# Kernel tuning notes

Hardware: AMD Instinct MI355X
Metric: run time of the kernel (lower is better)

Reference implementation:

```python
import jax, jax.numpy as jnp
import numpy as np

N = 50000          # nodes
E = 1_600_000      # directed edges (before self-loops)
F_IN = 256         # input features
HID = 32           # hidden channels
HEADS = 8
NUM_CLASSES = 40


def setup_inputs() -> dict:
    key = jax.random.key(0)
    ks = jax.random.split(key, 12)
    s = 0.1  # small init scale for numerical sanity
    return {
        "x": jax.random.normal(ks[0], (N, F_IN), jnp.float32),
        "edge_index": jax.random.randint(ks[1], (2, E), 0, N, dtype=jnp.int32),
        # layer 0: F_IN -> HID, heads=8, concat
        "W0": jax.random.normal(ks[2], (F_IN, HEADS * HID), jnp.float32) * s,
        "as0": jax.random.normal(ks[3], (HEADS, HID), jnp.float32) * s,
        "ad0": jax.random.normal(ks[4], (HEADS, HID), jnp.float32) * s,
        "b0": jnp.zeros((HEADS * HID,), jnp.float32),
        # layer 1: 8*HID -> 8*HID, heads=1, concat
        "W1": jax.random.normal(ks[5], (HEADS * HID, HEADS * HID), jnp.float32) * s,
        "as1": jax.random.normal(ks[6], (1, HEADS * HID), jnp.float32) * s,
        "ad1": jax.random.normal(ks[7], (1, HEADS * HID), jnp.float32) * s,
        "b1": jnp.zeros((HEADS * HID,), jnp.float32),
        # layer 2: 8*HID -> NUM_CLASSES, heads=1, concat=False (mean == identity for 1 head)
        "W2": jax.random.normal(ks[8], (HEADS * HID, NUM_CLASSES), jnp.float32) * s,
        "as2": jax.random.normal(ks[9], (1, NUM_CLASSES), jnp.float32) * s,
        "ad2": jax.random.normal(ks[10], (1, NUM_CLASSES), jnp.float32) * s,
        "b2": jnp.zeros((NUM_CLASSES,), jnp.float32),
    }


def _gat_conv(x, src, dst, W, att_src, att_dst, bias, heads, out_ch, concat):
    """PyG GATConv (eval mode, self-loops already included in src/dst)."""
    n = x.shape[0]
    xp = (x @ W).reshape(n, heads, out_ch)                # [N,H,C]
    a_src = jnp.einsum("nhc,hc->nh", xp, att_src)          # [N,H]
    a_dst = jnp.einsum("nhc,hc->nh", xp, att_dst)          # [N,H]
    e = jax.nn.leaky_relu(a_src[src] + a_dst[dst], 0.2)    # [Etot,H]
    # segment softmax over incoming edges of each destination node
    m = jax.ops.segment_max(e, dst, num_segments=n)        # [N,H]
    ex = jnp.exp(e - m[dst])
    denom = jax.ops.segment_sum(ex, dst, num_segments=n)   # [N,H]
    alpha = ex / denom[dst]                                # [Etot,H]
    msg = xp[src] * alpha[:, :, None]                      # [Etot,H,C]
    out = jax.ops.segment_sum(msg, dst, num_segments=n)    # [N,H,C]
    out = out.reshape(n, heads * out_ch) if concat else out.mean(axis=1)
    return out + bias


def reference(x, edge_index, W0, as0, ad0, b0, W1, as1, ad1, b1, W2, as2, ad2, b2):
    loops = jnp.arange(N, dtype=edge_index.dtype)
    src = jnp.concatenate([edge_index[0], loops])  # add self-loops (PyG default)
    dst = jnp.concatenate([edge_index[1], loops])
    h = _gat_conv(x, src, dst, W0, as0, ad0, b0, HEADS, HID, True)
    h = jax.nn.elu(h)  # dropout p=0.6 is identity in eval mode
    h = _gat_conv(h, src, dst, W1, as1, ad1, b1, 1, HEADS * HID, True)
    h = jax.nn.elu(h)
    x1 = _gat_conv(h, src, dst, W2, as2, ad2, b2, 1, NUM_CLASSES, False)
    return jax.nn.log_softmax(x1, axis=1)  # original returns log_softmax of last conv output
```

## Files before the change

### kernel.cpp

```cpp
#include <hip/hip_runtime.h>
#include <hip/hip_bf16.h>

#define N_NODES 50000
#define N_EDGES 1600000
#define ETOT (N_EDGES + N_NODES)
#define NP 50048
#define NBUCK 196

typedef __attribute__((ext_vector_type(8))) short short8;
typedef __attribute__((ext_vector_type(4))) float f32x4;
typedef __attribute__((ext_vector_type(2))) float f32x2;

__device__ __forceinline__ float b2f(unsigned short u) {
    union { unsigned int i; float f; } v; v.i = ((unsigned int)u) << 16; return v.f;
}
__device__ __forceinline__ unsigned short f2b(float f) {
    union { float f; unsigned int i; } v; v.f = f;
    unsigned int r = v.i + 0x7FFF + ((v.i >> 16) & 1);
    return (unsigned short)(r >> 16);
}
__device__ __forceinline__ unsigned char f2q(float f) {
    int r = __builtin_amdgcn_cvt_pk_fp8_f32(f, f, 0, false);
    return (unsigned char)(r & 0xFF);
}

__global__ void k_tb(const float* __restrict__ W, unsigned short* __restrict__ Wt,
                     int K, int C) {
    int idx = blockIdx.x * 256 + threadIdx.x;
    if (idx >= K * C) return;
    int k = idx / C, c = idx - k * C;
    Wt[c * K + k] = f2b(W[idx]);
}

__global__ __launch_bounds__(256) void k_mku0(const float* __restrict__ W,
                                              const float* __restrict__ attS,
                                              const float* __restrict__ attD,
                                              unsigned short* __restrict__ u0t) {
    int lane = threadIdx.x & 63;
    int k = blockIdx.x * 4 + (threadIdx.x >> 6);
    if (k >= 256) return;
    int h = lane >> 3, c0 = lane & 7;
    const float* wr = W + (size_t)k * 256 + h * 32;
    float ss = 0.f, sd = 0.f;
    #pragma unroll
    for (int t = 0; t < 4; ++t) {
        int c = c0 + t * 8;
        float w = wr[c];
        ss += w * attS[h * 32 + c];
        sd += w * attD[h * 32 + c];
    }
    #pragma unroll
    for (int off = 1; off < 8; off <<= 1) {
        ss += __shfl_xor(ss, off);
        sd += __shfl_xor(sd, off);
    }
    if (c0 == 0) {
        u0t[(size_t)h * 256 + k] = f2b(ss);
        u0t[(size_t)(8 + h) * 256 + k] = f2b(sd);
    }
}

__global__ __launch_bounds__(256) void k_mku1(const float* __restrict__ W,
                                              const float* __restrict__ attS,
                                              const float* __restrict__ attD,
                                              float* __restrict__ u, int C) {
    int lane = threadIdx.x & 63;
    int k = blockIdx.x * 4 + (threadIdx.x >> 6);
    if (k >= 256) return;
    const float* wr = W + (size_t)k * C;
    float ss = 0.f, sd = 0.f;
    for (int c = lane; c < C; c += 64) {
        float w = wr[c];
        ss += w * attS[c];
        sd += w * attD[c];
    }
    #pragma unroll
    for (int off = 32; off > 0; off >>= 1) {
        ss += __shfl_xor(ss, off);
        sd += __shfl_xor(sd, off);
    }
    if (lane == 0) { u[k * 2] = ss; u[k * 2 + 1] = sd; }
}

__global__ __launch_bounds__(256) void k_bcount(const int* __restrict__ ei,
                                                int* __restrict__ bcnt) {
    __shared__ int h[NBUCK];
    for (int i = threadIdx.x; i < NBUCK; i += 256) h[i] = 0;
    __syncthreads();
    int e0 = blockIdx.x * 4096, e1 = min(e0 + 4096, ETOT);
    for (int e = e0 + threadIdx.x; e < e1; e += 256) {
        int dst = (e < N_EDGES) ? ei[N_EDGES + e] : (e - N_EDGES);
        atomicAdd(&h[dst >> 8], 1);
    }
    __syncthreads();
    for (int i = threadIdx.x; i < NBUCK; i += 256)
        if (h[i]) atomicAdd(&bcnt[i], h[i]);
}

__global__ void k_bscan(const int* __restrict__ bcnt, int* __restrict__ bstart,
                        int* __restrict__ bcursor) {
    __shared__ int tmp[256];
    int t = threadIdx.x;
    int v = (t < NBUCK) ? bcnt[t] : 0;
    tmp[t] = v;
    __syncthreads();
    for (int off = 1; off < 256; off <<= 1) {
        int u = (t >= off) ? tmp[t - off] : 0;
        __syncthreads();
        tmp[t] += u;
        __syncthreads();
    }
    int ex = tmp[t] - v;
    if (t < NBUCK) { bstart[t] = ex; bcursor[t] = ex; }
    if (t == 0) bstart[NBUCK] = ETOT;
}

__global__ __launch_bounds__(256) void k_bscatter(const int* __restrict__ ei,
                                                  int* __restrict__ bcursor,
                                                  unsigned int* __restrict__ stage) {
    __shared__ int h[NBUCK], base[NBUCK], cur[NBUCK], gbase[NBUCK];
    __shared__ int tmp[256];
    __shared__ unsigned int buf[8192];
    int t = threadIdx.x;
    for (int i = t; i < NBUCK; i += 256) h[i] = 0;
    __syncthreads();
    int e0 = blockIdx.x * 8192, e1 = min(e0 + 8192, ETOT);
    for (int e = e0 + t; e < e1; e += 256) {
        int dst = (e < N_EDGES) ? ei[N_EDGES + e] : (e - N_EDGES);
        atomicAdd(&h[dst >> 8], 1);
    }
    __syncthreads();
    int v = (t < NBUCK) ? h[t] : 0;
    tmp[t] = v;
    __syncthreads();
    for (int off = 1; off < 256; off <<= 1) {
        int u = (t >= off) ? tmp[t - off] : 0;
        __syncthreads();
        tmp[t] += u;
        __syncthreads();
    }
    if (t < NBUCK) { base[t] = tmp[t] - v; cur[t] = tmp[t] - v; }
    __syncthreads();
    for (int e = e0 + t; e < e1; e += 256) {
        int src, dst;
        if (e < N_EDGES) { src = ei[e]; dst = ei[N_EDGES + e]; }
        else             { src = dst = e - N_EDGES; }
        int b = dst >> 8;
        int p = atomicAdd(&cur[b], 1);
        buf[p] = ((unsigned int)b << 24) | ((unsigned int)src << 8) | (unsigned int)(dst & 255);
    }
    __syncthreads();
    if (t < NBUCK) gbase[t] = atomicAdd(&bcursor[t], h[t]);
    __syncthreads();
    int cnt = e1 - e0;
    for (int i = t; i < cnt; i += 256) {
        unsigned int pr = buf[i];
        int b = pr >> 24;
        stage[gbase[b] + (i - base[b])] = pr;
    }
}

__global__ __launch_bounds__(256) void k_csr(const unsigned int* __restrict__ stage,
                                             const int* __restrict__ bstart,
                                             int* __restrict__ rowptr, int* __restrict__ deg,
                                             unsigned short* __restrict__ csr) {
    __shared__ int cnt[256], cur[256], tmp[256];
    int b = blockIdx.x;
    int t = threadIdx.x;
    cnt[t] = 0;
    __syncthreads();
    int s0 = bstart[b], s1 = bstart[b + 1];
    for (int i = s0 + t; i < s1; i += 256)
        atomicAdd(&cnt[stage[i] & 255], 1);
    __syncthreads();
    int v = cnt[t];
    tmp[t] = v;
    __syncthreads();
    for (int off = 1; off < 256; off <<= 1) {
        int u = (t >= off) ? tmp[t - off] : 0;
        __syncthreads();
        tmp[t] += u;
        __syncthreads();
    }
    int ex = tmp[t] - v;
    int node = b * 256 + t;
    if (node < N_NODES) { rowptr[node] = s0 + ex; deg[node] = v; }
    cur[t] = s0 + ex;
    __syncthreads();
    for (int i = s0 + t; i < s1; i += 256) {
        unsigned int pr = stage[i];
        int p = atomicAdd(&cur[pr & 255], 1);
        csr[p] = (unsigned short)((pr >> 8) & 0xFFFF);
    }
}

template <bool ATT>
__global__ __launch_bounds__(256) void k_gemm_w(
    const unsigned short* __restrict__ A, const unsigned short* __restrict__ Bt,
    unsigned char* __restrict__ Cout,
    const unsigned short* __restrict__ But,
    float* __restrict__ Catt,
    int nrows, int ldc) {
    const int K = 256;
    int lane = threadIdx.x & 63;
    int wave = threadIdx.x >> 6;
    int row0 = blockIdx.x * 128 + wave * 32;
    int col0 = blockIdx.y * 128;
    bool doAtt = ATT && (blockIdx.y == 0);
    int ar0 = row0 + (lane & 15); if (ar0 >= nrows) ar0 = nrows - 1;
    int ar1 = row0 + 16 + (lane & 15); if (ar1 >= nrows) ar1 = nrows - 1;
    int ks = (lane >> 4) * 8;
    const unsigned short* Ap0 = A + (size_t)ar0 * K + ks;
    const unsigned short* Ap1 = A + (size_t)ar1 * K + ks;
    f32x4 acc[2][8];
    f32x4 aat[2] = {{0,0,0,0},{0,0,0,0}};
    #pragma unroll
    for (int rt = 0; rt < 2; ++rt)
        #pragma unroll
        for (int ct = 0; ct < 8; ++ct) acc[rt][ct] = {0, 0, 0, 0};
    for (int k = 0; k < K; k += 32) {
        short8 a0 = *(const short8*)(Ap0 + k);
        short8 a1 = *(const short8*)(Ap1 + k);
        #pragma unroll
        for (int ct = 0; ct < 8; ++ct) {
            short8 b = *(const short8*)(Bt + (size_t)(col0 + ct * 16 + (lane & 15)) * K + k + ks);
            acc[0][ct] = __builtin_amdgcn_mfma_f32_16x16x32_bf16(a0, b, acc[0][ct], 0, 0, 0);
            acc[1][ct] = __builtin_amdgcn_mfma_f32_16x16x32_bf16(a1, b, acc[1][ct], 0, 0, 0);
        }
        if (doAtt) {
            short8 b = *(const short8*)(But + (size_t)(lane & 15) * K + k + ks);
            aat[0] = __builtin_amdgcn_mfma_f32_16x16x32_bf16(a0, b, aat[0], 0, 0, 0);
            aat[1] = __builtin_amdgcn_mfma_f32_16x16x32_bf16(a1, b, aat[1], 0, 0, 0);
        }
    }
    int cb = lane & 15;
    #pragma unroll
    for (int rt = 0; rt < 2; ++rt) {
        int rbase = row0 + rt * 16 + (lane >> 4) * 4;
        #pragma unroll
        for (int ct = 0; ct < 8; ++ct) {
            int cc = col0 + ct * 16 + cb;
            #pragma unroll
            for (int j = 0; j < 4; ++j)
                Cout[(size_t)(rbase + j) * ldc + cc] = f2q(acc[rt][ct][j]);
        }
        if (doAtt) {
            #pragma unroll
            for (int j = 0; j < 4; ++j)
                Catt[(size_t)(rbase + j) * 16 + cb] = aat[rt][j];
        }
    }
}

__global__ __launch_bounds__(256) void k_gemm_b(
    const unsigned short* __restrict__ A, const unsigned short* __restrict__ Bt,
    unsigned char* __restrict__ Cout, int nrows, int ncols, int ldc) {
    const int K = 256;
    int lane = threadIdx.x & 63;
    int wave = threadIdx.x >> 6;
    int row0 = blockIdx.x * 128 + wave * 32;
    int ar0 = row0 + (lane & 15); if (ar0 >= nrows) ar0 = nrows - 1;
    int ar1 = row0 + 16 + (lane & 15); if (ar1 >= nrows) ar1 = nrows - 1;
    int ks = (lane >> 4) * 8;
    const unsigned short* Ap0 = A + (size_t)ar0 * K + ks;
    const unsigned short* Ap1 = A + (size_t)ar1 * K + ks;
    f32x4 acc[2][4] = {{{0,0,0,0},{0,0,0,0},{0,0,0,0},{0,0,0,0}},
                       {{0,0,0,0},{0,0,0,0},{0,0,0,0},{0,0,0,0}}};
    for (int k = 0; k < K; k += 32) {
        short8 a0 = *(const short8*)(Ap0 + k);
        short8 a1 = *(const short8*)(Ap1 + k);
        #pragma unroll
        for (int ct = 0; ct < 4; ++ct) {
            short8 b = *(const short8*)(Bt + (size_t)(ct * 16 + (lane & 15)) * K + k + ks);
            acc[0][ct] = __builtin_amdgcn_mfma_f32_16x16x32_bf16(a0, b, acc[0][ct], 0, 0, 0);
            acc[1][ct] = __builtin_amdgcn_mfma_f32_16x16x32_bf16(a1, b, acc[1][ct], 0, 0, 0);
        }
    }
    int cb = lane & 15;
    #pragma unroll
    for (int rt = 0; rt < 2; ++rt) {
        int rbase = row0 + rt * 16 + (lane >> 4) * 4;
        #pragma unroll
        for (int ct = 0; ct < 4; ++ct) {
            int cc = ct * 16 + cb;
            #pragma unroll
            for (int j = 0; j < 4; ++j) {
                float v = (cc < ncols) ? acc[rt][ct][j] : 0.f;
                Cout[(size_t)(rbase + j) * ldc + cc] = f2q(v);
            }
        }
    }
}

__global__ __launch_bounds__(256) void k_split(const float* __restrict__ x,
                                               unsigned short* __restrict__ xb) {
    int idx = blockIdx.x * 256 + threadIdx.x;
    if (idx >= N_NODES * 64) return;
    float4 v = *(const float4*)(x + (size_t)idx * 4);
    ushort4 w;
    w.x = f2b(v.x); w.y = f2b(v.y); w.z = f2b(v.z); w.w = f2b(v.w);
    *(ushort4*)(xb + (size_t)idx * 4) = w;
}

template <int H>
__global__ __launch_bounds__(256) void k_gatherq(
    const unsigned char* __restrict__ xq,
    const float* __restrict__ asrc, const float* __restrict__ adst,
    const int* __restrict__ rowptr, const int* __restrict__ deg,
    const unsigned short* __restrict__ csr,
    const float* __restrict__ bias,
    const float* __restrict__ un,
    unsigned short* __restrict__ o,
    float* __restrict__ asn, float* __restrict__ adn) {
    constexpr int SS = (H == 8) ? 16 : 1;
    int lane = threadIdx.x & 63;
    int node = blockIdx.x * 4 + (threadIdx.x >> 6);
    if (node >= N_NODES) return;
    int ptr = rowptr[node], dg = deg[node];
    int g = lane >> 4, l4 = lane & 15;
    int cbase = l4 * 16;
    int head = (H == 8) ? (l4 >> 1) : 0;
    float ad = adst[(size_t)node * SS + head];
    float acc[16];
    #pragma unroll
    for (int j = 0; j < 16; ++j) acc[j] = 0.f;
    float den = 0.f;
    int dge = (dg + 3) & ~3;
    int i = g;
    int ci = ptr + min(i, dg - 1);
    int sn0 = csr[ci];
    float e0 = asrc[(size_t)sn0 * SS + head];
    uint4 v0 = *(const uint4*)(xq + (size_t)sn0 * 256 + cbase);
    bool ok0 = (i < dg);
    while (i < dge) {
        int in = i + 4;
        int cn = ptr + min(in, dg - 1);
        int sn1 = csr[cn];
        float e1 = asrc[(size_t)sn1 * SS + head];
        uint4 v1 = *(const uint4*)(xq + (size_t)sn1 * 256 + cbase);
        float e = e0 + ad;
        e = (e >= 0.f) ? e : 0.2f * e;
        float a0 = ok0 ? __expf(fminf(e, 70.f)) : 0.f;
        den += a0;
        f32x2 f;
        f = __builtin_amdgcn_cvt_pk_f32_fp8(v0.x, false); acc[0] += a0 * f.x;  acc[1] += a0 * f.y;
        f = __builtin_amdgcn_cvt_pk_f32_fp8(v0.x, true);  acc[2] += a0 * f.x;  acc[3] += a0 * f.y;
        f = __builtin_amdgcn_cvt_pk_f32_fp8(v0.y, false); acc[4] += a0 * f.x;  acc[5] += a0 * f.y;
        f = __builtin_amdgcn_cvt_pk_f32_fp8(v0.y, true);  acc[6] += a0 * f.x;  acc[7] += a0 * f.y;
        f = __builtin_amdgcn_cvt_pk_f32_fp8(v0.z, false); acc[8] += a0 * f.x;  acc[9] += a0 * f.y;
        f = __builtin_amdgcn_cvt_pk_f32_fp8(v0.z, true);  acc[10] += a0 * f.x; acc[11] += a0 * f.y;
        f = __builtin_amdgcn_cvt_pk_f32_fp8(v0.w, false); acc[12] += a0 * f.x; acc[13] += a0 * f.y;
        f = __builtin_amdgcn_cvt_pk_f32_fp8(v0.w, true);  acc[14] += a0 * f.x; acc[15] += a0 * f.y;
        i = in; e0 = e1; v0 = v1; ok0 = (in < dg);
    }
    den += __shfl_xor(den, 16);
    den += __shfl_xor(den, 32);
    #pragma unroll
    for (int j = 0; j < 16; ++j) {
        acc[j] += __shfl_xor(acc[j], 16);
        acc[j] += __shfl_xor(acc[j], 32);
    }
    if (g) return;
    float inv = 1.0f / den;
    float sN = 0.f, dN = 0.f;
    short8 w0, w1;
    #pragma unroll
    for (int j = 0; j < 16; ++j) {
        int c = cbase + j;
        float v = acc[j] * inv + bias[c];
        v = (v > 0.f) ? v : (__expf(v) - 1.f);
        unsigned short bb = f2b(v);
        if (j < 8) w0[j] = (short)bb; else w1[j - 8] = (short)bb;
        sN += v * un[c * 2];
        dN += v * un[c * 2 + 1];
    }
    *(short8*)(o + (size_t)node * 256 + cbase) = w0;
    *(short8*)(o + (size_t)node * 256 + cbase + 8) = w1;
    #pragma unroll
    for (int off = 8; off > 0; off >>= 1) {
        sN += __shfl_xor(sN, off);
        dN += __shfl_xor(dN, off);
    }
    if (l4 == 0) { asn[node] = sN; adn[node] = dN; }
}

__global__ __launch_bounds__(256) void k_gf(
    const unsigned char* __restrict__ xq,
    const float* __restrict__ asrc, const float* __restrict__ adst,
    const int* __restrict__ rowptr, const int* __restrict__ deg,
    const unsigned short* __restrict__ csr,
    const float* __restrict__ bias,
    float* __restrict__ out) {
    int lane = threadIdx.x & 63;
    int node = blockIdx.x * 4 + (threadIdx.x >> 6);
    if (node >= N_NODES) return;
    int ptr = rowptr[node], dg = deg[node];
    int g = lane >> 3, l8 = lane & 7;
    int cbase = l8 * 8;
    float ad = adst[node];
    float acc[8] = {0,0,0,0,0,0,0,0};
    float den = 0.f;
    int dge = (dg + 7) & ~7;
    int i = g;
    int ci = ptr + min(i, dg - 1);
    int sn0 = csr[ci];
    float e0 = asrc[sn0];
    uint2 v0 = *(const uint2*)(xq + (size_t)sn0 * 64 + cbase);
    bool ok0 = (i < dg);
    while (i < dge) {
        int in = i + 8;
        int cn = ptr + min(in, dg - 1);
        int sn1 = csr[cn];
        float e1 = asrc[sn1];
        uint2 v1 = *(const uint2*)(xq + (size_t)sn1 * 64 + cbase);
        float e = e0 + ad;
        e = (e >= 0.f) ? e : 0.2f * e;
        float a0 = ok0 ? __expf(fminf(e, 70.f)) : 0.f;
        den += a0;
        f32x2 f;
        f = __builtin_amdgcn_cvt_pk_f32_fp8(v0.x, false); acc[0] += a0 * f.x; acc[1] += a0 * f.y;
        f = __builtin_amdgcn_cvt_pk_f32_fp8(v0.x, true);  acc[2] += a0 * f.x; acc[3] += a0 * f.y;
        f = __builtin_amdgcn_cvt_pk_f32_fp8(v0.y, false); acc[4] += a0 * f.x; acc[5] += a0 * f.y;
        f = __builtin_amdgcn_cvt_pk_f32_fp8(v0.y, true);  acc[6] += a0 * f.x; acc[7] += a0 * f.y;
        i = in; e0 = e1; v0 = v1; ok0 = (in < dg);
    }
    den += __shfl_xor(den, 8);
    den += __shfl_xor(den, 16);
    den += __shfl_xor(den, 32);
    #pragma unroll
    for (int j = 0; j < 8; ++j) {
        acc[j] += __shfl_xor(acc[j], 8);
        acc[j] += __shfl_xor(acc[j], 16);
        acc[j] += __shfl_xor(acc[j], 32);
    }
    if (g) return;
    float inv = 1.0f / den;
    float val[8], mx = -1e30f;
    #pragma unroll
    for (int j = 0; j < 8; ++j) {
        int c = cbase + j;
        val[j] = (c < 40) ? acc[j] * inv + bias[c] : -1e30f;
        mx = fmaxf(mx, val[j]);
    }
    #pragma unroll
    for (int off = 4; off > 0; off >>= 1) mx = fmaxf(mx, __shfl_xor(mx, off));
    float ex = 0.f;
    #pragma unroll
    for (int j = 0; j < 8; ++j) {
        int c = cbase + j;
        if (c < 40) ex += __expf(val[j] - mx);
    }
    #pragma unroll
    for (int off = 4; off > 0; off >>= 1) ex += __shfl_xor(ex, off);
    float lse = __logf(ex);
    #pragma unroll
    for (int j = 0; j < 8; ++j) {
        int c = cbase + j;
        if (c < 40) out[(size_t)node * 40 + c] = val[j] - mx - lse;
    }
}

extern "C" void kernel_launch(void* const* d_in, const int* in_sizes, int n_in,
                              void* d_out, int out_size, void* d_ws, size_t ws_size,
                              hipStream_t stream) {
    const float* x   = (const float*)d_in[0];
    const int*   ei  = (const int*)d_in[1];
    const float* W0  = (const float*)d_in[2];
    const float* as0 = (const float*)d_in[3];
    const float* ad0 = (const float*)d_in[4];
    const float* b0  = (const float*)d_in[5];
    const float* W1  = (const float*)d_in[6];
    const float* as1 = (const float*)d_in[7];
    const float* ad1 = (const float*)d_in[8];
    const float* b1  = (const float*)d_in[9];
    const float* W2  = (const float*)d_in[10];
    const float* as2 = (const float*)d_in[11];
    const float* ad2 = (const float*)d_in[12];
    const float* b2  = (const float*)d_in[13];
    float* out = (float*)d_out;

    char* p = (char*)d_ws;
    auto carve = [&](size_t bytes) -> char* {
        char* r = p; p += (bytes + 255) & ~(size_t)255; return r;
    };
    unsigned short* xb   = (unsigned short*)carve((size_t)NP * 256 * 2);
    unsigned short* xpb  = (unsigned short*)carve((size_t)NP * 256 * 2);
    unsigned short* h    = (unsigned short*)carve((size_t)NP * 256 * 2);
    unsigned char*  xq2  = (unsigned char*)carve((size_t)NP * 64);
    unsigned short* Wt0  = (unsigned short*)carve(256 * 256 * 2);
    unsigned short* Wt1  = (unsigned short*)carve(256 * 256 * 2);
    unsigned short* Wt2  = (unsigned short*)carve(64 * 256 * 2);
    unsigned short* u0t  = (unsigned short*)carve(16 * 256 * 2);
    float* att0 = (float*)carve((size_t)NP * 16 * 4);
    float* u1 = (float*)carve(256 * 2 * 4);
    float* u2 = (float*)carve(256 * 2 * 4);
    float* asrc1 = (float*)carve((size_t)N_NODES * 4);
    float* adst1 = (float*)carve((size_t)N_NODES * 4);
    float* asrc2 = (float*)carve((size_t)N_NODES * 4);
    float* adst2 = (float*)carve((size_t)N_NODES * 4);
    int* deg    = (int*)carve((size_t)N_NODES * 4);
    int* rowptr = (int*)carve((size_t)N_NODES * 4);
    int* bcnt   = (int*)carve((size_t)NBUCK * 4);
    int* bstart = (int*)carve((size_t)(NBUCK + 1) * 4);
    int* bcursor= (int*)carve((size_t)NBUCK * 4);
    unsigned int* stage = (unsigned int*)carve((size_t)ETOT * 4);
    unsigned short* csr = (unsigned short*)carve((size_t)ETOT * 2);
    unsigned char* xq = (unsigned char*)xpb;

    hipMemsetAsync(bcnt, 0, (size_t)NBUCK * 4, stream);
    hipMemsetAsync(Wt2, 0, 64 * 256 * 2, stream);

    k_tb<<<(256 * 256 + 255) / 256, 256, 0, stream>>>(W0, Wt0, 256, 256);
    k_tb<<<(256 * 256 + 255) / 256, 256, 0, stream>>>(W1, Wt1, 256, 256);
    k_tb<<<(256 * 40 + 255) / 256, 256, 0, stream>>>(W2, Wt2, 256, 40);

    k_mku0<<<64, 256, 0, stream>>>(W0, as0, ad0, u0t);
    k_mku1<<<64, 256, 0, stream>>>(W1, as1, ad1, u1, 256);
    k_mku1<<<64, 256, 0, stream>>>(W2, as2, ad2, u2, 40);

    k_bcount<<<(ETOT + 4095) / 4096, 256, 0, stream>>>(ei, bcnt);
    k_bscan<<<1, 256, 0, stream>>>(bcnt, bstart, bcursor);
    k_bscatter<<<(ETOT + 8191) / 8192, 256, 0, stream>>>(ei, bcursor, stage);
    k_csr<<<NBUCK, 256, 0, stream>>>(stage, bstart, rowptr, deg, csr);

    dim3 gg(NP / 128, 2);
    dim3 gn(N_NODES / 4);
    dim3 g1(NP / 128);
    k_split<<<(N_NODES * 64 + 255) / 256, 256, 0, stream>>>(x, xb);
    k_gemm_w<true><<<gg, 256, 0, stream>>>(xb, Wt0, xq, u0t, att0, N_NODES, 256);
    k_gatherq<8><<<gn, 256, 0, stream>>>(xq, att0, att0 + 8, rowptr, deg, csr,
                                         b0, u1, h, asrc1, adst1);
    k_gemm_w<false><<<gg, 256, 0, stream>>>(h, Wt1, xq, nullptr, nullptr, N_NODES, 256);
    k_gatherq<1><<<gn, 256, 0, stream>>>(xq, asrc1, adst1, rowptr, deg, csr,
                                         b1, u2, xb, asrc2, adst2);
    k_gemm_b<<<g1, 256, 0, stream>>>(xb, Wt2, xq2, N_NODES, 40, 64);
    k_gf<<<gn, 256, 0, stream>>>(xq2, asrc2, adst2, rowptr, deg, csr, b2, out);
}
```

Measured before the change: 412.1 us.

## Use fixed-capacity buckets to drop count/scan passes and merge setup kernels

```diff
diff --git a/kernel.cpp b/kernel.cpp
--- a/kernel.cpp
+++ b/kernel.cpp
@@ -6,6 +6,7 @@
 #define ETOT (N_EDGES + N_NODES)
 #define NP 50048
 #define NBUCK 196
+#define BCAP 16384
 
 typedef __attribute__((ext_vector_type(8))) short short8;
 typedef __attribute__((ext_vector_type(4))) float f32x4;
@@ -24,12 +25,24 @@
     return (unsigned char)(r & 0xFF);
 }
 
-__global__ void k_tb(const float* __restrict__ W, unsigned short* __restrict__ Wt,
-                     int K, int C) {
+__global__ void k_tb3(const float* __restrict__ W0, const float* __restrict__ W1,
+                      const float* __restrict__ W2,
+                      unsigned short* __restrict__ Wt0, unsigned short* __restrict__ Wt1,
+                      unsigned short* __restrict__ Wt2) {
     int idx = blockIdx.x * 256 + threadIdx.x;
-    if (idx >= K * C) return;
-    int k = idx / C, c = idx - k * C;
-    Wt[c * K + k] = f2b(W[idx]);
+    if (idx < 65536) {
+        int k = idx >> 8, c = idx & 255;
+        Wt0[c * 256 + k] = f2b(W0[idx]);
+    } else if (idx < 131072) {
+        int i = idx - 65536;
+        int k = i >> 8, c = i & 255;
+        Wt1[c * 256 + k] = f2b(W1[i]);
+    } else {
+        int i = idx - 131072;
+        if (i >= 16384) return;
+        int k = i >> 6, c = i & 63;
+        Wt2[c * 256 + k] = (c < 40) ? f2b(W2[k * 40 + c]) : 0;
+    }
 }
 
 __global__ __launch_bounds__(256) void k_mku0(const float* __restrict__ W,
@@ -60,19 +73,26 @@
     }
 }
 
-__global__ __launch_bounds__(256) void k_mku1(const float* __restrict__ W,
-                                              const float* __restrict__ attS,
-                                              const float* __restrict__ attD,
-                                              float* __restrict__ u, int C) {
+__global__ __launch_bounds__(256) void k_mku1x2(const float* __restrict__ W1,
+                                                const float* __restrict__ as1,
+                                                const float* __restrict__ ad1,
+                                                const float* __restrict__ W2,
+                                                const float* __restrict__ as2,
+                                                const float* __restrict__ ad2,
+                                                float* __restrict__ u1,
+                                                float* __restrict__ u2) {
     int lane = threadIdx.x & 63;
-    int k = blockIdx.x * 4 + (threadIdx.x >> 6);
-    if (k >= 256) return;
+    int r = blockIdx.x * 4 + (threadIdx.x >> 6);
+    if (r >= 512) return;
+    const float* W; const float* aS; const float* aD; float* u; int C, k;
+    if (r < 256) { W = W1; aS = as1; aD = ad1; u = u1; C = 256; k = r; }
+    else         { W = W2; aS = as2; aD = ad2; u = u2; C = 40;  k = r - 256; }
     const float* wr = W + (size_t)k * C;
     float ss = 0.f, sd = 0.f;
     for (int c = lane; c < C; c += 64) {
         float w = wr[c];
-        ss += w * attS[c];
-        sd += w * attD[c];
+        ss += w * aS[c];
+        sd += w * aD[c];
     }
     #pragma unroll
     for (int off = 32; off > 0; off >>= 1) {
@@ -82,41 +102,8 @@
     if (lane == 0) { u[k * 2] = ss; u[k * 2 + 1] = sd; }
 }
 
-__global__ __launch_bounds__(256) void k_bcount(const int* __restrict__ ei,
-                                                int* __restrict__ bcnt) {
-    __shared__ int h[NBUCK];
-    for (int i = threadIdx.x; i < NBUCK; i += 256) h[i] = 0;
-    __syncthreads();
-    int e0 = blockIdx.x * 4096, e1 = min(e0 + 4096, ETOT);
-    for (int e = e0 + threadIdx.x; e < e1; e += 256) {
-        int dst = (e < N_EDGES) ? ei[N_EDGES + e] : (e - N_EDGES);
-        atomicAdd(&h[dst >> 8], 1);
-    }
-    __syncthreads();
-    for (int i = threadIdx.x; i < NBUCK; i += 256)
-        if (h[i]) atomicAdd(&bcnt[i], h[i]);
-}
-
-__global__ void k_bscan(const int* __restrict__ bcnt, int* __restrict__ bstart,
-                        int* __restrict__ bcursor) {
-    __shared__ int tmp[256];
-    int t = threadIdx.x;
-    int v = (t < NBUCK) ? bcnt[t] : 0;
-    tmp[t] = v;
-    __syncthreads();
-    for (int off = 1; off < 256; off <<= 1) {
-        int u = (t >= off) ? tmp[t - off] : 0;
-        __syncthreads();
-        tmp[t] += u;
-        __syncthreads();
-    }
-    int ex = tmp[t] - v;
-    if (t < NBUCK) { bstart[t] = ex; bcursor[t] = ex; }
-    if (t == 0) bstart[NBUCK] = ETOT;
-}
-
 __global__ __launch_bounds__(256) void k_bscatter(const int* __restrict__ ei,
-                                                  int* __restrict__ bcursor,
+                                                  int* __restrict__ bcnt,
                                                   unsigned int* __restrict__ stage) {
     __shared__ int h[NBUCK], base[NBUCK], cur[NBUCK], gbase[NBUCK];
     __shared__ int tmp[256];
@@ -150,7 +137,7 @@
         buf[p] = ((unsigned int)b << 24) | ((unsigned int)src << 8) | (unsigned int)(dst & 255);
     }
     __syncthreads();
-    if (t < NBUCK) gbase[t] = atomicAdd(&bcursor[t], h[t]);
+    if (t < NBUCK) gbase[t] = t * BCAP + atomicAdd(&bcnt[t], h[t]);
     __syncthreads();
     int cnt = e1 - e0;
     for (int i = t; i < cnt; i += 256) {
@@ -161,7 +148,7 @@
 }
 
 __global__ __launch_bounds__(256) void k_csr(const unsigned int* __restrict__ stage,
-                                             const int* __restrict__ bstart,
+                                             const int* __restrict__ bcnt,
                                              int* __restrict__ rowptr, int* __restrict__ deg,
                                              unsigned short* __restrict__ csr) {
     __shared__ int cnt[256], cur[256], tmp[256];
@@ -169,7 +156,7 @@
     int t = threadIdx.x;
     cnt[t] = 0;
     __syncthreads();
-    int s0 = bstart[b], s1 = bstart[b + 1];
+    int s0 = b * BCAP, s1 = s0 + bcnt[b];
     for (int i = s0 + t; i < s1; i += 256)
         atomicAdd(&cnt[stage[i] & 255], 1);
     __syncthreads();
@@ -501,27 +488,18 @@
     int* deg    = (int*)carve((size_t)N_NODES * 4);
     int* rowptr = (int*)carve((size_t)N_NODES * 4);
     int* bcnt   = (int*)carve((size_t)NBUCK * 4);
-    int* bstart = (int*)carve((size_t)(NBUCK + 1) * 4);
-    int* bcursor= (int*)carve((size_t)NBUCK * 4);
-    unsigned int* stage = (unsigned int*)carve((size_t)ETOT * 4);
-    unsigned short* csr = (unsigned short*)carve((size_t)ETOT * 2);
+    unsigned int* stage = (unsigned int*)carve((size_t)NBUCK * BCAP * 4);
+    unsigned short* csr = (unsigned short*)carve((size_t)NBUCK * BCAP * 2);
     unsigned char* xq = (unsigned char*)xpb;
 
     hipMemsetAsync(bcnt, 0, (size_t)NBUCK * 4, stream);
-    hipMemsetAsync(Wt2, 0, 64 * 256 * 2, stream);
-
-    k_tb<<<(256 * 256 + 255) / 256, 256, 0, stream>>>(W0, Wt0, 256, 256);
-    k_tb<<<(256 * 256 + 255) / 256, 256, 0, stream>>>(W1, Wt1, 256, 256);
-    k_tb<<<(256 * 40 + 255) / 256, 256, 0, stream>>>(W2, Wt2, 256, 40);
-
+
+    k_tb3<<<(147456 + 255) / 256, 256, 0, stream>>>(W0, W1, W2, Wt0, Wt1, Wt2);
     k_mku0<<<64, 256, 0, stream>>>(W0, as0, ad0, u0t);
-    k_mku1<<<64, 256, 0, stream>>>(W1, as1, ad1, u1, 256);
-    k_mku1<<<64, 256, 0, stream>>>(W2, as2, ad2, u2, 40);
-
-    k_bcount<<<(ETOT + 4095) / 4096, 256, 0, stream>>>(ei, bcnt);
-    k_bscan<<<1, 256, 0, stream>>>(bcnt, bstart, bcursor);
-    k_bscatter<<<(ETOT + 8191) / 8192, 256, 0, stream>>>(ei, bcursor, stage);
-    k_csr<<<NBUCK, 256, 0, stream>>>(stage, bstart, rowptr, deg, csr);
+    k_mku1x2<<<128, 256, 0, stream>>>(W1, as1, ad1, W2, as2, ad2, u1, u2);
+
+    k_bscatter<<<(ETOT + 8191) / 8192, 256, 0, stream>>>(ei, bcnt, stage);
+    k_csr<<<NBUCK, 256, 0, stream>>>(stage, bcnt, rowptr, deg, csr);
 
     dim3 gg(NP / 128, 2);
     dim3 gn(N_NODES / 4);
```

Result: faster. 389.7 us (-5.4%).
